# Kernel optimization log

Measured on AMD Instinct MI355X. Metric: run time of the kernel, lower is better.

Reference implementation:

```python
import jax, jax.numpy as jnp
import numpy as np

B, T, S, SYM, FFT = 256, 4, 2, 14, 128   # batch, num_tx, streams_per_tx, ofdm symbols, fft size
NSC, GUARD = 108, 10                      # effective subcarriers, guard offset
L = SYM * NSC                             # 1512, de-mash matrix dimension


def setup_inputs() -> dict:
    key = jax.random.key(0)
    k1, k2, k3, k4 = jax.random.split(key, 4)
    scale = 1.0 / np.sqrt(L).astype(np.float32)  # keep C roughly unitary-scaled
    return {
        "x_real": jax.random.normal(k1, (B, T, S, SYM, FFT), jnp.float32),
        "x_imag": jax.random.normal(k2, (B, T, S, SYM, FFT), jnp.float32),
        "C_real": jax.random.normal(k3, (L, L), jnp.float32) * scale,
        "C_imag": jax.random.normal(k4, (L, L), jnp.float32) * scale,
        "sc_ind": jnp.arange(NSC, dtype=jnp.int32) + GUARD,  # effective subcarrier indices
    }


def reference(x_real, x_imag, C_real, C_imag, sc_ind):
    # Complex RG and de-mash matrix
    x = jax.lax.complex(x_real, x_imag)           # [B,T,S,SYM,FFT] complex64
    C = jax.lax.complex(C_real, C_imag)           # [L,L] complex64

    # gather effective subcarriers along last axis
    y = jnp.take(x, sc_ind, axis=-1)              # [B,T,S,SYM,NSC]
    b, t, s, sym, nsc = y.shape

    # flatten_last_dims(y, 2) and multiply from right by C^H (adjoint=True)
    yf = y.reshape(b, t, s, sym * nsc)            # [B,T,S,L]
    yf = jnp.einsum('btsl,ml->btsm', yf, jnp.conj(C))  # y @ C^H
    y = yf.reshape(b, t, s, sym, nsc)             # [B,T,S,SYM,NSC]

    # scatter back into the full grid (equivalent to the transpose/scatter_nd/transpose chain,
    # since sc_ind is unique and the scatter is along the subcarrier axis)
    out = jnp.zeros(x.shape, x.dtype).at[..., sc_ind].set(y)

    # return real/imag stacked so the output is a single float32 array
    return jnp.stack([out.real, out.imag], axis=0)  # [2,B,T,S,SYM,FFT]
```

## Files before the change

### kernel.cpp

```cpp
#include <hip/hip_runtime.h>
#include <cstdint>
#include <cstddef>


typedef _Float16 half_t;
typedef half_t half8 __attribute__((ext_vector_type(8)));
typedef half_t half4 __attribute__((ext_vector_type(4)));
typedef half_t half2_t __attribute__((ext_vector_type(2)));
typedef float floatx4 __attribute__((ext_vector_type(4)));
typedef float floatv4 __attribute__((ext_vector_type(4)));

#define M_DIM 2048
#define N_DIM 3072
#define K_DIM 3072
#define LDIM 1512
#define NSC 108
#define SYMS 14
#define FFT 128
#define ROWLEN (SYMS * FFT)

#define BM 64
#define BN 128
#define BK 64
#define NITER (K_DIM / BK)

#define PA2_BLOCKS 6048
#define PW2_BLOCKS 9072
#define PAP_BLOCKS 48
#define PG_BLOCKS 4480
#define PREP_BLOCKS (PA2_BLOCKS + PW2_BLOCKS + PAP_BLOCKS + PG_BLOCKS)

typedef __attribute__((address_space(3))) uint32_t lds_u32_t;
typedef const __attribute__((address_space(1))) uint32_t glob_u32_t;

__device__ __forceinline__ void gl2lds16(const void* g, void* l) {
    __builtin_amdgcn_global_load_lds((glob_u32_t*)g, (lds_u32_t*)l, 16, 0, 0);
}

__global__ __launch_bounds__(256) void prep_all(
    const float* __restrict__ xr, const float* __restrict__ xi,
    const float* __restrict__ Cr, const float* __restrict__ Ci,
    const int* __restrict__ sc,
    half_t* __restrict__ A, half_t* __restrict__ W, float* __restrict__ out)
{
    const int b = blockIdx.x;
    const int t = threadIdx.x;

    if (b < PA2_BLOCKS) {
        int idx = b * 256 + t;
        int jp = idx % 54;
        int rest = idx / 54;
        int sym = rest % 14;
        int row = rest / 14;
        int s0 = sc[2 * jp];
        int s1 = sc[2 * jp + 1];
        const float* xrp = xr + (size_t)row * ROWLEN + sym * FFT;
        const float* xip = xi + (size_t)row * ROWLEN + sym * FFT;
        half2_t hr = { (half_t)xrp[s0], (half_t)xrp[s1] };
        half2_t hi = { (half_t)xip[s0], (half_t)xip[s1] };
        size_t dst = (size_t)row * K_DIM + sym * NSC + 2 * jp;
        *(half2_t*)(A + dst) = hr;
        *(half2_t*)(A + dst + LDIM) = hi;
    } else if (b < PA2_BLOCKS + PW2_BLOCKS) {
        int idx = (b - PA2_BLOCKS) * 256 + t;
        int kq = idx % 756;
        int n = idx / 756;
        int k0 = kq * 4;
        floatv4 f = {0.0f, 0.0f, 0.0f, 0.0f};
        if (n < LDIM) {
            if (k0 < LDIM)
                f = *(const floatv4*)(Cr + (size_t)n * LDIM + k0);
            else
                f = *(const floatv4*)(Ci + (size_t)n * LDIM + (k0 - LDIM));
        } else if (n < 2 * LDIM) {
            int m = n - LDIM;
            if (k0 < LDIM) {
                f = *(const floatv4*)(Ci + (size_t)m * LDIM + k0);
                f = -f;
            } else {
                f = *(const floatv4*)(Cr + (size_t)m * LDIM + (k0 - LDIM));
            }
        }
        half4 h = { (half_t)f.x, (half_t)f.y, (half_t)f.z, (half_t)f.w };
        *(half4*)(W + (size_t)n * K_DIM + k0) = h;
    } else if (b < PA2_BLOCKS + PW2_BLOCKS + PAP_BLOCKS) {
        int idx = (b - PA2_BLOCKS - PW2_BLOCKS) * 256 + t;
        int c = idx % 6;
        int row = idx / 6;
        half8 z = {};
        *(half8*)(A + (size_t)row * K_DIM + 2 * LDIM + c * 8) = z;
    } else {
        int idx = (b - PA2_BLOCKS - PW2_BLOCKS - PAP_BLOCKS) * 256 + t;
        int c20 = idx % 20;
        int rest = idx / 20;
        int sym = rest % 14;
        int rowri = rest / 14;
        int col = (c20 < 10) ? c20 : (NSC + c20);
        out[(size_t)rowri * ROWLEN + sym * FFT + col] = 0.0f;
    }
}

__global__ __launch_bounds__(256) void gemm_scatter(
    const half_t* __restrict__ A,
    const half_t* __restrict__ W,
    const int* __restrict__ sc,
    float* __restrict__ out)
{
    __shared__ __align__(16) half_t As[BM * BK];
    __shared__ __align__(16) half_t Bs[BN * BK];

    const int t = threadIdx.x;

    const int blk = blockIdx.x;
    const int xcd = blk & 7;
    const int j = blk >> 3;
    const int bn = xcd * 3 + (j % 3);
    const int bm = j / 3;

    const int lane = t & 63;
    const int wn = (t >> 6) * 32;

    floatx4 acc[4][2] = {};

    const half_t* gAp[2];
    const half_t* gBp[4];
    half_t* lAp[2];
    half_t* lBp[4];
#pragma unroll
    for (int r = 0; r < 2; ++r) {
        int c = r * 256 + t;
        int row = c >> 3, slot = c & 7;
        int g = slot ^ (row & 7);
        gAp[r] = A + (size_t)(bm * BM + row) * K_DIM + g * 8;
        lAp[r] = As + c * 8;
    }
#pragma unroll
    for (int r = 0; r < 4; ++r) {
        int c = r * 256 + t;
        int row = c >> 3, slot = c & 7;
        int g = slot ^ (row & 7);
        gBp[r] = W + (size_t)(bn * BN + row) * K_DIM + g * 8;
        lBp[r] = Bs + c * 8;
    }

    const int fr = lane & 15;
    const int cr = lane >> 4;
    const int slot0 = (cr) ^ (fr & 7);
    const int slot1 = (4 + cr) ^ (fr & 7);

    for (int kb = 0; kb < NITER; ++kb) {
        __syncthreads();
        gl2lds16(gAp[0], lAp[0]);
        gl2lds16(gAp[1], lAp[1]);
        gl2lds16(gBp[0], lBp[0]);
        gl2lds16(gBp[1], lBp[1]);
        gl2lds16(gBp[2], lBp[2]);
        gl2lds16(gBp[3], lBp[3]);
        gAp[0] += BK; gAp[1] += BK;
        gBp[0] += BK; gBp[1] += BK; gBp[2] += BK; gBp[3] += BK;
        __syncthreads();

        half8 af[2][4], bf[2][2];
#pragma unroll
        for (int i = 0; i < 4; ++i) {
            int rbase = (i * 16 + fr) * BK;
            af[0][i] = *(const half8*)&As[rbase + slot0 * 8];
            af[1][i] = *(const half8*)&As[rbase + slot1 * 8];
        }
#pragma unroll
        for (int j2 = 0; j2 < 2; ++j2) {
            int rbase = (wn + j2 * 16 + fr) * BK;
            bf[0][j2] = *(const half8*)&Bs[rbase + slot0 * 8];
            bf[1][j2] = *(const half8*)&Bs[rbase + slot1 * 8];
        }
#pragma unroll
        for (int s = 0; s < 2; ++s)
#pragma unroll
            for (int i = 0; i < 4; ++i)
#pragma unroll
                for (int j2 = 0; j2 < 2; ++j2)
                    acc[i][j2] = __builtin_amdgcn_mfma_f32_16x16x32_f16(
                        af[s][i], bf[s][j2], acc[i][j2], 0, 0, 0);
    }

    const int col_base = bn * BN + wn + (lane & 15);
    const int row_base = bm * BM + ((lane >> 4) * 4);
#pragma unroll
    for (int j2 = 0; j2 < 2; ++j2) {
        int n = col_base + j2 * 16;
        if (n >= 2 * LDIM) continue;
        int ri = (n >= LDIM) ? 1 : 0;
        int nn = n - ri * LDIM;
        int sym = nn / NSC;
        int jj = nn - sym * NSC;
        size_t colOff = (size_t)ri * (M_DIM * ROWLEN) + sym * FFT + sc[jj];
#pragma unroll
        for (int i = 0; i < 4; ++i) {
            int row0 = row_base + i * 16;
#pragma unroll
            for (int r = 0; r < 4; ++r) {
                out[colOff + (size_t)(row0 + r) * ROWLEN] = acc[i][j2][r];
            }
        }
    }
}

extern "C" void kernel_launch(void* const* d_in, const int* in_sizes, int n_in,
                              void* d_out, int out_size, void* d_ws, size_t ws_size,
                              hipStream_t stream) {
    const float* xr = (const float*)d_in[0];
    const float* xi = (const float*)d_in[1];
    const float* Cr = (const float*)d_in[2];
    const float* Ci = (const float*)d_in[3];
    const int* sc   = (const int*)d_in[4];
    float* out = (float*)d_out;

    half_t* Ah = (half_t*)d_ws;
    half_t* Wh = (half_t*)((char*)d_ws + (size_t)M_DIM * K_DIM * 2);

    prep_all<<<PREP_BLOCKS, 256, 0, stream>>>(
        xr, xi, Cr, Ci, sc, Ah, Wh, out);

    gemm_scatter<<<768, 256, 0, stream>>>(Ah, Wh, sc, out);
}
```

Before: 154.5 us.

## Split GEMM K dimension in two with atomic accumulation into zeroed output

```diff
diff --git a/kernel.cpp b/kernel.cpp
--- a/kernel.cpp
+++ b/kernel.cpp
@@ -22,13 +22,14 @@
 #define BM 64
 #define BN 128
 #define BK 64
-#define NITER (K_DIM / BK)
+#define KSPLIT 2
+#define NITER_S (K_DIM / BK / KSPLIT)
 
 #define PA2_BLOCKS 6048
 #define PW2_BLOCKS 9072
 #define PAP_BLOCKS 48
-#define PG_BLOCKS 4480
-#define PREP_BLOCKS (PA2_BLOCKS + PW2_BLOCKS + PAP_BLOCKS + PG_BLOCKS)
+#define PZ_BLOCKS 7168
+#define PREP_BLOCKS (PA2_BLOCKS + PW2_BLOCKS + PAP_BLOCKS + PZ_BLOCKS)
 
 typedef __attribute__((address_space(3))) uint32_t lds_u32_t;
 typedef const __attribute__((address_space(1))) uint32_t glob_u32_t;
@@ -91,12 +92,8 @@
         *(half8*)(A + (size_t)row * K_DIM + 2 * LDIM + c * 8) = z;
     } else {
         int idx = (b - PA2_BLOCKS - PW2_BLOCKS - PAP_BLOCKS) * 256 + t;
-        int c20 = idx % 20;
-        int rest = idx / 20;
-        int sym = rest % 14;
-        int rowri = rest / 14;
-        int col = (c20 < 10) ? c20 : (NSC + c20);
-        out[(size_t)rowri * ROWLEN + sym * FFT + col] = 0.0f;
+        floatv4 z = {0.0f, 0.0f, 0.0f, 0.0f};
+        *(floatv4*)(out + (size_t)idx * 4) = z;
     }
 }
 
@@ -110,12 +107,14 @@
     __shared__ __align__(16) half_t Bs[BN * BK];
 
     const int t = threadIdx.x;
-
     const int blk = blockIdx.x;
-    const int xcd = blk & 7;
-    const int j = blk >> 3;
-    const int bn = xcd * 3 + (j % 3);
-    const int bm = j / 3;
+    const int kz = blk >> 9 ? 0 : 0;
+    const int kzz = blk / 768;
+    const int rest = blk - kzz * 768;
+    const int bn = rest % 24;
+    const int bm = rest / 24;
+    const int kofs = kzz * (K_DIM / KSPLIT);
+    (void)kz;
 
     const int lane = t & 63;
     const int wn = (t >> 6) * 32;
@@ -131,7 +130,7 @@
         int c = r * 256 + t;
         int row = c >> 3, slot = c & 7;
         int g = slot ^ (row & 7);
-        gAp[r] = A + (size_t)(bm * BM + row) * K_DIM + g * 8;
+        gAp[r] = A + (size_t)(bm * BM + row) * K_DIM + kofs + g * 8;
         lAp[r] = As + c * 8;
     }
 #pragma unroll
@@ -139,7 +138,7 @@
         int c = r * 256 + t;
         int row = c >> 3, slot = c & 7;
         int g = slot ^ (row & 7);
-        gBp[r] = W + (size_t)(bn * BN + row) * K_DIM + g * 8;
+        gBp[r] = W + (size_t)(bn * BN + row) * K_DIM + kofs + g * 8;
         lBp[r] = Bs + c * 8;
     }
 
@@ -148,7 +147,7 @@
     const int slot0 = (cr) ^ (fr & 7);
     const int slot1 = (4 + cr) ^ (fr & 7);
 
-    for (int kb = 0; kb < NITER; ++kb) {
+    for (int kb = 0; kb < NITER_S; ++kb) {
         __syncthreads();
         gl2lds16(gAp[0], lAp[0]);
         gl2lds16(gAp[1], lAp[1]);
@@ -199,7 +198,8 @@
             int row0 = row_base + i * 16;
 #pragma unroll
             for (int r = 0; r < 4; ++r) {
-                out[colOff + (size_t)(row0 + r) * ROWLEN] = acc[i][j2][r];
+                unsafeAtomicAdd(&out[colOff + (size_t)(row0 + r) * ROWLEN],
+                                acc[i][j2][r]);
             }
         }
     }
@@ -221,5 +221,5 @@
     prep_all<<<PREP_BLOCKS, 256, 0, stream>>>(
         xr, xi, Cr, Ci, sc, Ah, Wh, out);
 
-    gemm_scatter<<<768, 256, 0, stream>>>(Ah, Wh, sc, out);
-}
+    gemm_scatter<<<768 * KSPLIT, 256, 0, stream>>>(Ah, Wh, sc, out);
+}
```

Result: slower. 215.9 us (+39.8%).

## Load B fragments directly from global into registers with double buffering

Applied to the files above, without the earlier changes.

```diff
diff --git a/kernel.cpp b/kernel.cpp
--- a/kernel.cpp
+++ b/kernel.cpp
@@ -100,32 +100,24 @@
     }
 }
 
-__global__ __launch_bounds__(256) void gemm_scatter(
+__global__ __launch_bounds__(256, 3) void gemm_scatter(
     const half_t* __restrict__ A,
     const half_t* __restrict__ W,
     const int* __restrict__ sc,
     float* __restrict__ out)
 {
     __shared__ __align__(16) half_t As[BM * BK];
-    __shared__ __align__(16) half_t Bs[BN * BK];
 
     const int t = threadIdx.x;
-
-    const int blk = blockIdx.x;
-    const int xcd = blk & 7;
-    const int j = blk >> 3;
-    const int bn = xcd * 3 + (j % 3);
-    const int bm = j / 3;
-
+    const int bn = blockIdx.x;
+    const int bm = blockIdx.y;
     const int lane = t & 63;
     const int wn = (t >> 6) * 32;
 
     floatx4 acc[4][2] = {};
 
     const half_t* gAp[2];
-    const half_t* gBp[4];
     half_t* lAp[2];
-    half_t* lBp[4];
 #pragma unroll
     for (int r = 0; r < 2; ++r) {
         int c = r * 256 + t;
@@ -134,33 +126,39 @@
         gAp[r] = A + (size_t)(bm * BM + row) * K_DIM + g * 8;
         lAp[r] = As + c * 8;
     }
-#pragma unroll
-    for (int r = 0; r < 4; ++r) {
-        int c = r * 256 + t;
-        int row = c >> 3, slot = c & 7;
-        int g = slot ^ (row & 7);
-        gBp[r] = W + (size_t)(bn * BN + row) * K_DIM + g * 8;
-        lBp[r] = Bs + c * 8;
-    }
 
     const int fr = lane & 15;
     const int cr = lane >> 4;
     const int slot0 = (cr) ^ (fr & 7);
     const int slot1 = (4 + cr) ^ (fr & 7);
 
+    const half_t* wp0 = W + (size_t)(bn * BN + wn + fr) * K_DIM + cr * 8;
+    const half_t* wp1 = wp0 + (size_t)16 * K_DIM;
+
+    half8 bf[2][2][2];
+    bf[0][0][0] = *(const half8*)(wp0);
+    bf[0][0][1] = *(const half8*)(wp1);
+    bf[0][1][0] = *(const half8*)(wp0 + 32);
+    bf[0][1][1] = *(const half8*)(wp1 + 32);
+
     for (int kb = 0; kb < NITER; ++kb) {
+        const int par = kb & 1;
         __syncthreads();
         gl2lds16(gAp[0], lAp[0]);
         gl2lds16(gAp[1], lAp[1]);
-        gl2lds16(gBp[0], lBp[0]);
-        gl2lds16(gBp[1], lBp[1]);
-        gl2lds16(gBp[2], lBp[2]);
-        gl2lds16(gBp[3], lBp[3]);
         gAp[0] += BK; gAp[1] += BK;
-        gBp[0] += BK; gBp[1] += BK; gBp[2] += BK; gBp[3] += BK;
         __syncthreads();
 
-        half8 af[2][4], bf[2][2];
+        if (kb + 1 < NITER) {
+            const half_t* b0 = wp0 + (kb + 1) * BK;
+            const half_t* b1 = wp1 + (kb + 1) * BK;
+            bf[par ^ 1][0][0] = *(const half8*)(b0);
+            bf[par ^ 1][0][1] = *(const half8*)(b1);
+            bf[par ^ 1][1][0] = *(const half8*)(b0 + 32);
+            bf[par ^ 1][1][1] = *(const half8*)(b1 + 32);
+        }
+
+        half8 af[2][4];
 #pragma unroll
         for (int i = 0; i < 4; ++i) {
             int rbase = (i * 16 + fr) * BK;
@@ -168,19 +166,13 @@
             af[1][i] = *(const half8*)&As[rbase + slot1 * 8];
         }
 #pragma unroll
-        for (int j2 = 0; j2 < 2; ++j2) {
-            int rbase = (wn + j2 * 16 + fr) * BK;
-            bf[0][j2] = *(const half8*)&Bs[rbase + slot0 * 8];
-            bf[1][j2] = *(const half8*)&Bs[rbase + slot1 * 8];
-        }
-#pragma unroll
         for (int s = 0; s < 2; ++s)
 #pragma unroll
             for (int i = 0; i < 4; ++i)
 #pragma unroll
                 for (int j2 = 0; j2 < 2; ++j2)
                     acc[i][j2] = __builtin_amdgcn_mfma_f32_16x16x32_f16(
-                        af[s][i], bf[s][j2], acc[i][j2], 0, 0, 0);
+                        af[s][i], bf[par][s][j2], acc[i][j2], 0, 0, 0);
     }
 
     const int col_base = bn * BN + wn + (lane & 15);
@@ -221,5 +213,6 @@
     prep_all<<<PREP_BLOCKS, 256, 0, stream>>>(
         xr, xi, Cr, Ci, sc, Ah, Wh, out);
 
-    gemm_scatter<<<768, 256, 0, stream>>>(Ah, Wh, sc, out);
-}
+    dim3 grid(N_DIM / BN, M_DIM / BM);
+    gemm_scatter<<<grid, 256, 0, stream>>>(Ah, Wh, sc, out);
+}
```

New measurement: 190.1 us. 1.23x slower.
